# Kernel tuning notes

Measured on AMD Instinct MI355X. Metric: run time of the kernel, lower is better.

Reference implementation:

```python
import jax, jax.numpy as jnp
import numpy as np

B, H, S, D = 2, 16, 2048, 64  # depth = dmodel / num_heads
DMODEL = H * D


def setup_inputs() -> dict:
    key = jax.random.key(0)
    kq, kk, kv, kw = jax.random.split(key, 4)
    Q = jax.random.normal(kq, (B, H, S, D), dtype=jnp.float32)
    K = jax.random.normal(kk, (B, H, S, D), dtype=jnp.float32)
    V = jax.random.normal(kv, (B, H, S, D), dtype=jnp.float32)
    W = jax.random.normal(kw, (DMODEL, DMODEL), dtype=jnp.float32) * (1.0 / np.sqrt(DMODEL))
    b = jnp.zeros((DMODEL,), dtype=jnp.float32)
    return {"Q": Q, "K": K, "V": V, "W": W, "b": b}


def reference(Q, K, V, W, b):
    depth = Q.shape[-1]
    # scores: (B, H, S, S) -- full score matrix, matching the original math
    scores = jnp.einsum('bhqd,bhkd->bhqk', Q, K) / jnp.sqrt(jnp.float32(depth))
    attn = jax.nn.softmax(scores, axis=-1)
    vals = jnp.einsum('bhqk,bhkd->bhqd', attn, V)          # (B, H, S, D)
    vals = jnp.transpose(vals, (0, 2, 1, 3))               # (B, S, H, D)
    concat = vals.reshape(vals.shape[0], vals.shape[1], -1)  # (B, S, dmodel)
    return concat @ W + b
```

## Files before the change

kernel.cpp:

```cpp
#include <hip/hip_runtime.h>
#include <hip/hip_bf16.h>


typedef float  f32x16 __attribute__((ext_vector_type(16)));
typedef float  f32x4v __attribute__((ext_vector_type(4)));
typedef float  f32x2v __attribute__((ext_vector_type(2)));
typedef __bf16 bf16x8 __attribute__((ext_vector_type(8)));
typedef __bf16 bf16x4 __attribute__((ext_vector_type(4)));
typedef __bf16 bf16x2 __attribute__((ext_vector_type(2)));

static constexpr int Bn = 2, Hn = 16, Sn = 2048, Dn = 64, DM = 1024;
static constexpr size_t QKV_ELEMS = (size_t)Bn * Hn * Sn * Dn;

#define QSCALE 0.18033688011112042f

#define LGKM_BARRIER() do {                                  \
    asm volatile("s_waitcnt lgkmcnt(0)" ::: "memory");       \
    __builtin_amdgcn_s_barrier();                            \
  } while (0)

#if __has_builtin(__builtin_amdgcn_cvt_pk_bf16_f32)
static __device__ __forceinline__ unsigned pack2(float a, float b) {
  bf16x2 t = __builtin_amdgcn_cvt_pk_bf16_f32(a, b);
  union { bf16x2 v; unsigned u; } c; c.v = t; return c.u;
}
#else
static __device__ __forceinline__ unsigned pack2(float a, float b) {
  union { __bf16 h; unsigned short s; } ua, ub;
  ua.h = (__bf16)a; ub.h = (__bf16)b;
  return (unsigned)ua.s | ((unsigned)ub.s << 16);
}
#endif

static __device__ __forceinline__ void unzip8(const unsigned* wds, bf16x8* r0, bf16x8* r1) {
  union { unsigned u[4]; bf16x8 v; } a, b;
#pragma unroll
  for (int i = 0; i < 4; ++i) {
    unsigned lo = wds[2 * i], hi = wds[2 * i + 1];
    a.u[i] = (lo & 0xffffu) | (hi << 16);
    b.u[i] = (lo >> 16) | (hi & 0xffff0000u);
  }
  *r0 = a.v; *r1 = b.v;
}

__global__ __launch_bounds__(256) void convert_vw(
    const float* __restrict__ v, const float* __restrict__ w,
    __bf16* __restrict__ vt, __bf16* __restrict__ wt) {
  __shared__ __bf16 T[64][74];
  const int bid = blockIdx.x, t = threadIdx.x;

  const float* s0;
  __bf16* dst0 = nullptr;
  int nt_ = 0, kt_ = 0;
  const bool isW = (bid >= 1024);
  {
    const int r = t >> 2, c0 = (t & 3) * 16;
    if (!isW) {
      const int idx = bid;
      const int kv0 = (idx & 31) * 64, bh = idx >> 5;
      s0 = v + ((size_t)bh * Sn + kv0 + r) * Dn + c0;
      dst0 = vt + (size_t)bh * Dn * Sn + kv0;
    } else {
      const int idx = bid - 1024;
      nt_ = (idx & 15) * 64; kt_ = (idx >> 4) * 64;
      s0 = w + (size_t)(kt_ + r) * DM + nt_ + c0;
    }
    union { bf16x8 v8; unsigned u[4]; } o0, o1;
#pragma unroll
    for (int i = 0; i < 2; ++i) {
      f32x4v f = *(const f32x4v*)(s0 + i * 4);
#pragma unroll
      for (int j = 0; j < 4; ++j) o0.v8[i * 4 + j] = (__bf16)f[j];
    }
#pragma unroll
    for (int i = 0; i < 2; ++i) {
      f32x4v f = *(const f32x4v*)(s0 + 8 + i * 4);
#pragma unroll
      for (int j = 0; j < 4; ++j) o1.v8[i * 4 + j] = (__bf16)f[j];
    }
#pragma unroll
    for (int j = 0; j < 4; ++j) {
      *(unsigned*)&T[r][c0 + 2 * j]     = o0.u[j];
      *(unsigned*)&T[r][c0 + 8 + 2 * j] = o1.u[j];
    }
  }
  __syncthreads();
  const int rp = t >> 3, k0 = (t & 7) * 8;
  unsigned wds[8];
#pragma unroll
  for (int i = 0; i < 8; ++i) wds[i] = *(const unsigned*)&T[k0 + i][2 * rp];
  bf16x8 r0, r1; unzip8(wds, &r0, &r1);
  if (!isW) {
    __bf16* d0 = dst0 + (size_t)(2 * rp) * Sn + k0;
    *(bf16x8*)d0 = r0;
    *(bf16x8*)(d0 + Sn) = r1;
  } else {
    const int n0 = nt_ + 2 * rp;
    __bf16* d0 = wt + ((size_t)(n0 >> 5) * 128 + (kt_ >> 3) + (t & 7)) * 256
                    + (n0 & 31) * 8;
    *(bf16x8*)d0 = r0;
    *(bf16x8*)(d0 + 8) = r1;
  }
}

__global__ __launch_bounds__(512, 4) void attn(
    const float* __restrict__ Qf, const float* __restrict__ Kf,
    const __bf16* __restrict__ Vtg, __bf16* __restrict__ Cc, int bz) {
  const int tid = threadIdx.x;
  const int wave = tid >> 6, lane = tid & 63;
  const int ln = lane & 31, g = lane >> 5;
  const int qg = wave >> 1, kh = wave & 1;
  const int f = blockIdx.x;
  const int swz = (f & 7) * 32 + (f >> 3);
  const int qb = swz & 15, h = swz >> 4;

  __shared__ __bf16 Ks[2][128][72];
  __shared__ __bf16 Vs[2][64][136];

  const size_t hoff = (size_t)(bz * Hn + h) * Sn * Dn;
  const float*  Qp = Qf + hoff + (size_t)(qb * 128 + qg * 32) * Dn;
  const float*  Kp = Kf + hoff;
  const __bf16* Vp = Vtg + hoff;

  bf16x8 qf[4];
#pragma unroll
  for (int ks = 0; ks < 4; ++ks) {
    const float* qp = Qp + (size_t)ln * Dn + ks * 16 + g * 8;
    f32x4v f0 = *(const f32x4v*)qp;
    f32x4v f1 = *(const f32x4v*)(qp + 4);
#pragma unroll
    for (int j = 0; j < 4; ++j) {
      qf[ks][j]     = (__bf16)(f0[j] * QSCALE);
      qf[ks][4 + j] = (__bf16)(f1[j] * QSCALE);
    }
  }

  const int kr = tid >> 2, kc = (tid & 3) * 16;
  const int vr = tid >> 3, vc = (tid & 7) * 16;
  const float*  kbasef = Kp + (size_t)kr * Dn + kc;
  const __bf16* vbase  = Vp + (size_t)vr * Sn + vc;

  f32x4v ka0, ka1, ka2, ka3;
  bf16x8 v0r, v1r;
  {
    ka0 = *(const f32x4v*)(kbasef);
    ka1 = *(const f32x4v*)(kbasef + 4);
    ka2 = *(const f32x4v*)(kbasef + 8);
    ka3 = *(const f32x4v*)(kbasef + 12);
    bf16x8 kx0, kx1;
#pragma unroll
    for (int j = 0; j < 4; ++j) {
      kx0[j] = (__bf16)ka0[j]; kx0[4 + j] = (__bf16)ka1[j];
      kx1[j] = (__bf16)ka2[j]; kx1[4 + j] = (__bf16)ka3[j];
    }
    *(bf16x8*)&Ks[0][kr][kc]     = kx0;
    *(bf16x8*)&Ks[0][kr][kc + 8] = kx1;
    v0r = *(const bf16x8*)vbase; v1r = *(const bf16x8*)(vbase + 8);
    union { bf16x8 v; bf16x4 h[2]; } u0, u1; u0.v = v0r; u1.v = v1r;
    union { bf16x4 h[2]; bf16x8 v; } w0, w1;
    w0.h[0] = u0.h[0]; w0.h[1] = u1.h[0];
    w1.h[0] = u0.h[1]; w1.h[1] = u1.h[1];
    *(bf16x8*)&Vs[0][vr][vc]     = w0.v;
    *(bf16x8*)&Vs[0][vr][vc + 8] = w1.v;
  }
  ka0 = *(const f32x4v*)(kbasef + (size_t)128 * Dn);
  ka1 = *(const f32x4v*)(kbasef + (size_t)128 * Dn + 4);
  ka2 = *(const f32x4v*)(kbasef + (size_t)128 * Dn + 8);
  ka3 = *(const f32x4v*)(kbasef + (size_t)128 * Dn + 12);
  v0r = *(const bf16x8*)(vbase + 128);
  v1r = *(const bf16x8*)(vbase + 128 + 8);
  LGKM_BARRIER();

  f32x16 O0 = {}, O1 = {};
  float Lown = 0.0f;
  constexpr int NT = Sn / 128;

  for (int kt = 0; kt < NT; ++kt) {
    const int buf = kt & 1;

    unsigned w[16];
#pragma unroll
    for (int m = 0; m < 2; ++m) {
      bf16x8 kf[4];
#pragma unroll
      for (int ks = 0; ks < 4; ++ks)
        kf[ks] = *(const bf16x8*)&Ks[buf][kh * 64 + m * 32 + ln][ks * 16 + g * 8];

      f32x16 s = {};
      __builtin_amdgcn_s_setprio(1);
#pragma unroll
      for (int ks = 0; ks < 4; ++ks)
        s = __builtin_amdgcn_mfma_f32_32x32x16_bf16(kf[ks], qf[ks], s, 0, 0, 0);
      __builtin_amdgcn_s_setprio(0);

      float p[16];
#pragma unroll
      for (int r = 0; r < 16; ++r) p[r] = __builtin_amdgcn_exp2f(s[r]);
      f32x2v s2 = {0.0f, 0.0f};
#pragma unroll
      for (int tt = 0; tt < 8; ++tt) { f32x2v t2 = {p[2 * tt], p[2 * tt + 1]}; s2 += t2; }
      Lown += s2[0] + s2[1];
#pragma unroll
      for (int tt = 0; tt < 8; ++tt) w[m * 8 + tt] = pack2(p[2 * tt], p[2 * tt + 1]);
    }

    if (kt + 1 < NT) {
      const int nb = buf ^ 1;
      bf16x8 kx0, kx1;
#pragma unroll
      for (int j = 0; j < 4; ++j) {
        kx0[j] = (__bf16)ka0[j]; kx0[4 + j] = (__bf16)ka1[j];
        kx1[j] = (__bf16)ka2[j]; kx1[4 + j] = (__bf16)ka3[j];
      }
      *(bf16x8*)&Ks[nb][kr][kc]     = kx0;
      *(bf16x8*)&Ks[nb][kr][kc + 8] = kx1;
      union { bf16x8 v; bf16x4 h[2]; } u0, u1; u0.v = v0r; u1.v = v1r;
      union { bf16x4 h[2]; bf16x8 v; } w0, w1;
      w0.h[0] = u0.h[0]; w0.h[1] = u1.h[0];
      w1.h[0] = u0.h[1]; w1.h[1] = u1.h[1];
      *(bf16x8*)&Vs[nb][vr][vc]     = w0.v;
      *(bf16x8*)&Vs[nb][vr][vc + 8] = w1.v;
      if (kt + 2 < NT) {
        const float* kp = kbasef + (size_t)(kt + 2) * 128 * Dn;
        ka0 = *(const f32x4v*)kp;       ka1 = *(const f32x4v*)(kp + 4);
        ka2 = *(const f32x4v*)(kp + 8); ka3 = *(const f32x4v*)(kp + 12);
        const __bf16* vp = vbase + (kt + 2) * 128;
        v0r = *(const bf16x8*)vp; v1r = *(const bf16x8*)(vp + 8);
      }
    }

    __builtin_amdgcn_s_setprio(1);
#pragma unroll
    for (int s4 = 0; s4 < 4; ++s4) {
      const int cb = kh * 64 + s4 * 16 + g * 8;
      bf16x8 vf0 = *(const bf16x8*)&Vs[buf][ln][cb];
      bf16x8 vf1 = *(const bf16x8*)&Vs[buf][32 + ln][cb];
      union { unsigned u[4]; bf16x8 v; } pu;
      pu.u[0] = w[s4 * 4 + 0];
      pu.u[1] = w[s4 * 4 + 1];
      pu.u[2] = w[s4 * 4 + 2];
      pu.u[3] = w[s4 * 4 + 3];
      O0 = __builtin_amdgcn_mfma_f32_32x32x16_bf16(vf0, pu.v, O0, 0, 0, 0);
      O1 = __builtin_amdgcn_mfma_f32_32x32x16_bf16(vf1, pu.v, O1, 0, 0, 0);
    }
    __builtin_amdgcn_s_setprio(0);

    LGKM_BARRIER();
  }

  const float Lred = Lown + __shfl_xor(Lown, 32);
  float* Ex = (float*)Ks;
  const int slot = (qg * 64 + lane) * 36;
  if (kh == 1) {
#pragma unroll
    for (int i = 0; i < 4; ++i) {
      f32x4v t = {O0[4 * i], O0[4 * i + 1], O0[4 * i + 2], O0[4 * i + 3]};
      *(f32x4v*)&Ex[slot + 4 * i] = t;
    }
#pragma unroll
    for (int i = 0; i < 4; ++i) {
      f32x4v t = {O1[4 * i], O1[4 * i + 1], O1[4 * i + 2], O1[4 * i + 3]};
      *(f32x4v*)&Ex[slot + 16 + 4 * i] = t;
    }
    Ex[slot + 32] = Lred;
  }
  __syncthreads();
  __bf16* T = (__bf16*)Vs;
  if (kh == 0) {
    float inv;
#pragma unroll
    for (int i = 0; i < 4; ++i) {
      f32x4v t = *(const f32x4v*)&Ex[slot + 4 * i];
#pragma unroll
      for (int c = 0; c < 4; ++c) O0[4 * i + c] += t[c];
    }
#pragma unroll
    for (int i = 0; i < 4; ++i) {
      f32x4v t = *(const f32x4v*)&Ex[slot + 16 + 4 * i];
#pragma unroll
      for (int c = 0; c < 4; ++c) O1[4 * i + c] += t[c];
    }
    inv = 1.0f / (Lred + Ex[slot + 32]);
#pragma unroll
    for (int dh = 0; dh < 2; ++dh) {
#pragma unroll
      for (int a = 0; a < 4; ++a) {
        const f32x16 O = dh ? O1 : O0;
        bf16x4 t4;
#pragma unroll
        for (int c = 0; c < 4; ++c) t4[c] = (__bf16)(O[4 * a + c] * inv);
        *(bf16x4*)&T[(qg * 32 + ln) * 72 + dh * 32 + 8 * a + 4 * g] = t4;
      }
    }
  }
  __syncthreads();
  const int q0 = qb * 128;
#pragma unroll
  for (int i = 0; i < 2; ++i) {
    const int rq = i * 64 + (tid >> 3);
    const int c8 = (tid & 7) * 8;
    bf16x8 o = *(const bf16x8*)&T[rq * 72 + c8];
    const int m = bz * Sn + q0 + rq;
    const int kg = h * 8 + (tid & 7);
    size_t base = ((size_t)(m >> 5) * 128 + kg) * 256 + (m & 31) * 8;
    *(bf16x8*)&Cc[base] = o;
  }
}

__global__ __launch_bounds__(512, 4) void proj(
    const __bf16* __restrict__ A2, const __bf16* __restrict__ Wt2,
    const float* __restrict__ bias, float* __restrict__ out) {
  const int tid = threadIdx.x, wave = tid >> 6, lane = tid & 63;
  const int ln = lane & 31, g = lane >> 5;
  const int mq = wave >> 1, nh = wave & 1;
  const int f = blockIdx.x;
  const int idx = f >> 3;
  const int bn = idx & 15;
  const int bm = (f & 7) * 4 + (idx >> 4);

  const int mg = bm * 4 + mq;
  const int ng = bn * 2 + nh;
  const __bf16* Ab = A2  + (size_t)mg * 128 * 256 + (size_t)ln * 8;
  const __bf16* Wb = Wt2 + (size_t)ng * 128 * 256 + (size_t)ln * 8;

  f32x16 acc = {};
#pragma unroll 4
  for (int kt = 0; kt < 16; ++kt) {
#pragma unroll
    for (int ks = 0; ks < 4; ++ks) {
      const size_t off = (size_t)(kt * 8 + ks * 2 + g) * 256;
      bf16x8 af = *(const bf16x8*)(Ab + off);
      bf16x8 wf = *(const bf16x8*)(Wb + off);
      acc = __builtin_amdgcn_mfma_f32_32x32x16_bf16(af, wf, acc, 0, 0, 0);
    }
  }
  const float bv = bias[bn * 64 + nh * 32 + ln];
#pragma unroll
  for (int r = 0; r < 16; ++r) {
    int row = bm * 128 + mq * 32 + (r & 3) + 8 * (r >> 2) + 4 * g;
    out[(size_t)row * DM + bn * 64 + nh * 32 + ln] = acc[r] + bv;
  }
}

extern "C" void kernel_launch(void* const* d_in, const int* in_sizes, int n_in,
                              void* d_out, int out_size, void* d_ws, size_t ws_size,
                              hipStream_t stream) {
  const float* Q = (const float*)d_in[0];
  const float* K = (const float*)d_in[1];
  const float* V = (const float*)d_in[2];
  const float* W = (const float*)d_in[3];
  const float* b = (const float*)d_in[4];
  float* out = (float*)d_out;

  __bf16* ws  = (__bf16*)d_ws;
  __bf16* Vtg = ws;
  __bf16* Cc  = Vtg + QKV_ELEMS;
  __bf16* Wt  = Cc + QKV_ELEMS;

  convert_vw<<<dim3(1280, 1, 1), 256, 0, stream>>>(V, W, Vtg, Wt);
  attn<<<dim3(256, 1, 1), 512, 0, stream>>>(Q, K, Vtg, Cc, 0);
  attn<<<dim3(256, 1, 1), 512, 0, stream>>>(Q, K, Vtg, Cc, 1);
  proj<<<dim3(512, 1, 1), 512, 0, stream>>>(Cc, Wt, b, out);
}
```

Measured before the change: 165.1 us.

## Process two query sub-tiles per wave and merge batch launches into one grid

Each wave now computes two 32-row query sub-tiles against the same K/V fragments read from LDS. The block shrinks to 256 threads (4 waves) while still covering 128 queries, so each K and V LDS load is reused across twice as many queries. The two per-batch attention launches become a single 512-block launch with the batch index taken from the block index, removing one launch and its tail. In exchange each wave holds more accumulators and Q fragments, so register pressure rises and occupancy may fall (launch bounds change to 256,2).

```diff
diff --git a/kernel.cpp b/kernel.cpp
--- a/kernel.cpp
+++ b/kernel.cpp
@@ -103,129 +103,156 @@
   }
 }
 
-__global__ __launch_bounds__(512, 4) void attn(
+__global__ __launch_bounds__(256, 2) void attn(
     const float* __restrict__ Qf, const float* __restrict__ Kf,
-    const __bf16* __restrict__ Vtg, __bf16* __restrict__ Cc, int bz) {
+    const __bf16* __restrict__ Vtg, __bf16* __restrict__ Cc) {
   const int tid = threadIdx.x;
   const int wave = tid >> 6, lane = tid & 63;
   const int ln = lane & 31, g = lane >> 5;
   const int qg = wave >> 1, kh = wave & 1;
   const int f = blockIdx.x;
-  const int swz = (f & 7) * 32 + (f >> 3);
-  const int qb = swz & 15, h = swz >> 4;
+  const int swz = (f & 7) * 64 + (f >> 3);
+  const int qb = swz & 15, h = (swz >> 4) & 15, bz = swz >> 8;
 
   __shared__ __bf16 Ks[2][128][72];
   __shared__ __bf16 Vs[2][64][136];
 
   const size_t hoff = (size_t)(bz * Hn + h) * Sn * Dn;
-  const float*  Qp = Qf + hoff + (size_t)(qb * 128 + qg * 32) * Dn;
+  const float*  Qp = Qf + hoff + (size_t)(qb * 128 + qg * 64) * Dn;
   const float*  Kp = Kf + hoff;
   const __bf16* Vp = Vtg + hoff;
 
-  bf16x8 qf[4];
-#pragma unroll
-  for (int ks = 0; ks < 4; ++ks) {
-    const float* qp = Qp + (size_t)ln * Dn + ks * 16 + g * 8;
-    f32x4v f0 = *(const f32x4v*)qp;
-    f32x4v f1 = *(const f32x4v*)(qp + 4);
-#pragma unroll
-    for (int j = 0; j < 4; ++j) {
-      qf[ks][j]     = (__bf16)(f0[j] * QSCALE);
-      qf[ks][4 + j] = (__bf16)(f1[j] * QSCALE);
-    }
-  }
-
-  const int kr = tid >> 2, kc = (tid & 3) * 16;
-  const int vr = tid >> 3, vc = (tid & 7) * 16;
-  const float*  kbasef = Kp + (size_t)kr * Dn + kc;
+  bf16x8 qf[2][4];
+#pragma unroll
+  for (int qs = 0; qs < 2; ++qs) {
+#pragma unroll
+    for (int ks = 0; ks < 4; ++ks) {
+      const float* qp = Qp + (size_t)(qs * 32 + ln) * Dn + ks * 16 + g * 8;
+      f32x4v f0 = *(const f32x4v*)qp;
+      f32x4v f1 = *(const f32x4v*)(qp + 4);
+#pragma unroll
+      for (int j = 0; j < 4; ++j) {
+        qf[qs][ks][j]     = (__bf16)(f0[j] * QSCALE);
+        qf[qs][ks][4 + j] = (__bf16)(f1[j] * QSCALE);
+      }
+    }
+  }
+
+  const int kra = tid >> 2, kc = (tid & 3) * 16;
+  const int vr  = tid >> 2, vc = (tid & 3) * 32;
+  const float*  kbasef = Kp + (size_t)kra * Dn + kc;
   const __bf16* vbase  = Vp + (size_t)vr * Sn + vc;
 
-  f32x4v ka0, ka1, ka2, ka3;
-  bf16x8 v0r, v1r;
+  f32x4v ka[2][4];
+  bf16x8 vld[4];
+#pragma unroll
+  for (int j = 0; j < 4; ++j) {
+    ka[0][j] = *(const f32x4v*)(kbasef + j * 4);
+    ka[1][j] = *(const f32x4v*)(kbasef + (size_t)64 * Dn + j * 4);
+  }
+#pragma unroll
+  for (int i = 0; i < 4; ++i) vld[i] = *(const bf16x8*)(vbase + i * 8);
   {
-    ka0 = *(const f32x4v*)(kbasef);
-    ka1 = *(const f32x4v*)(kbasef + 4);
-    ka2 = *(const f32x4v*)(kbasef + 8);
-    ka3 = *(const f32x4v*)(kbasef + 12);
-    bf16x8 kx0, kx1;
-#pragma unroll
-    for (int j = 0; j < 4; ++j) {
-      kx0[j] = (__bf16)ka0[j]; kx0[4 + j] = (__bf16)ka1[j];
-      kx1[j] = (__bf16)ka2[j]; kx1[4 + j] = (__bf16)ka3[j];
-    }
-    *(bf16x8*)&Ks[0][kr][kc]     = kx0;
-    *(bf16x8*)&Ks[0][kr][kc + 8] = kx1;
-    v0r = *(const bf16x8*)vbase; v1r = *(const bf16x8*)(vbase + 8);
-    union { bf16x8 v; bf16x4 h[2]; } u0, u1; u0.v = v0r; u1.v = v1r;
-    union { bf16x4 h[2]; bf16x8 v; } w0, w1;
+#pragma unroll
+    for (int r = 0; r < 2; ++r) {
+      bf16x8 kx0, kx1;
+#pragma unroll
+      for (int j = 0; j < 4; ++j) {
+        kx0[j] = (__bf16)ka[r][0][j]; kx0[4 + j] = (__bf16)ka[r][1][j];
+        kx1[j] = (__bf16)ka[r][2][j]; kx1[4 + j] = (__bf16)ka[r][3][j];
+      }
+      *(bf16x8*)&Ks[0][kra + r * 64][kc]     = kx0;
+      *(bf16x8*)&Ks[0][kra + r * 64][kc + 8] = kx1;
+    }
+    union { bf16x8 v; bf16x4 h[2]; } u0, u1, u2, u3;
+    u0.v = vld[0]; u1.v = vld[1]; u2.v = vld[2]; u3.v = vld[3];
+    union { bf16x4 h[2]; bf16x8 v; } w0, w1, w2, w3;
     w0.h[0] = u0.h[0]; w0.h[1] = u1.h[0];
     w1.h[0] = u0.h[1]; w1.h[1] = u1.h[1];
-    *(bf16x8*)&Vs[0][vr][vc]     = w0.v;
-    *(bf16x8*)&Vs[0][vr][vc + 8] = w1.v;
-  }
-  ka0 = *(const f32x4v*)(kbasef + (size_t)128 * Dn);
-  ka1 = *(const f32x4v*)(kbasef + (size_t)128 * Dn + 4);
-  ka2 = *(const f32x4v*)(kbasef + (size_t)128 * Dn + 8);
-  ka3 = *(const f32x4v*)(kbasef + (size_t)128 * Dn + 12);
-  v0r = *(const bf16x8*)(vbase + 128);
-  v1r = *(const bf16x8*)(vbase + 128 + 8);
+    w2.h[0] = u2.h[0]; w2.h[1] = u3.h[0];
+    w3.h[0] = u2.h[1]; w3.h[1] = u3.h[1];
+    *(bf16x8*)&Vs[0][vr][vc]      = w0.v;
+    *(bf16x8*)&Vs[0][vr][vc + 8]  = w1.v;
+    *(bf16x8*)&Vs[0][vr][vc + 16] = w2.v;
+    *(bf16x8*)&Vs[0][vr][vc + 24] = w3.v;
+  }
+#pragma unroll
+  for (int j = 0; j < 4; ++j) {
+    ka[0][j] = *(const f32x4v*)(kbasef + (size_t)128 * Dn + j * 4);
+    ka[1][j] = *(const f32x4v*)(kbasef + (size_t)192 * Dn + j * 4);
+  }
+#pragma unroll
+  for (int i = 0; i < 4; ++i) vld[i] = *(const bf16x8*)(vbase + 128 + i * 8);
   LGKM_BARRIER();
 
-  f32x16 O0 = {}, O1 = {};
-  float Lown = 0.0f;
+  f32x16 O[2][2] = {};
+  float Lown[2] = {0.0f, 0.0f};
   constexpr int NT = Sn / 128;
 
   for (int kt = 0; kt < NT; ++kt) {
     const int buf = kt & 1;
 
-    unsigned w[16];
+    unsigned w[2][16];
 #pragma unroll
     for (int m = 0; m < 2; ++m) {
       bf16x8 kf[4];
 #pragma unroll
       for (int ks = 0; ks < 4; ++ks)
         kf[ks] = *(const bf16x8*)&Ks[buf][kh * 64 + m * 32 + ln][ks * 16 + g * 8];
-
-      f32x16 s = {};
-      __builtin_amdgcn_s_setprio(1);
-#pragma unroll
-      for (int ks = 0; ks < 4; ++ks)
-        s = __builtin_amdgcn_mfma_f32_32x32x16_bf16(kf[ks], qf[ks], s, 0, 0, 0);
-      __builtin_amdgcn_s_setprio(0);
-
-      float p[16];
-#pragma unroll
-      for (int r = 0; r < 16; ++r) p[r] = __builtin_amdgcn_exp2f(s[r]);
-      f32x2v s2 = {0.0f, 0.0f};
-#pragma unroll
-      for (int tt = 0; tt < 8; ++tt) { f32x2v t2 = {p[2 * tt], p[2 * tt + 1]}; s2 += t2; }
-      Lown += s2[0] + s2[1];
-#pragma unroll
-      for (int tt = 0; tt < 8; ++tt) w[m * 8 + tt] = pack2(p[2 * tt], p[2 * tt + 1]);
+#pragma unroll
+      for (int qs = 0; qs < 2; ++qs) {
+        f32x16 s = {};
+        __builtin_amdgcn_s_setprio(1);
+#pragma unroll
+        for (int ks = 0; ks < 4; ++ks)
+          s = __builtin_amdgcn_mfma_f32_32x32x16_bf16(kf[ks], qf[qs][ks], s, 0, 0, 0);
+        __builtin_amdgcn_s_setprio(0);
+        float p[16];
+#pragma unroll
+        for (int r = 0; r < 16; ++r) p[r] = __builtin_amdgcn_exp2f(s[r]);
+        f32x2v s2 = {0.0f, 0.0f};
+#pragma unroll
+        for (int tt = 0; tt < 8; ++tt) { f32x2v t2 = {p[2 * tt], p[2 * tt + 1]}; s2 += t2; }
+        Lown[qs] += s2[0] + s2[1];
+#pragma unroll
+        for (int tt = 0; tt < 8; ++tt) w[qs][m * 8 + tt] = pack2(p[2 * tt], p[2 * tt + 1]);
+      }
     }
 
     if (kt + 1 < NT) {
       const int nb = buf ^ 1;
-      bf16x8 kx0, kx1;
-#pragma unroll
-      for (int j = 0; j < 4; ++j) {
-        kx0[j] = (__bf16)ka0[j]; kx0[4 + j] = (__bf16)ka1[j];
-        kx1[j] = (__bf16)ka2[j]; kx1[4 + j] = (__bf16)ka3[j];
-      }
-      *(bf16x8*)&Ks[nb][kr][kc]     = kx0;
-      *(bf16x8*)&Ks[nb][kr][kc + 8] = kx1;
-      union { bf16x8 v; bf16x4 h[2]; } u0, u1; u0.v = v0r; u1.v = v1r;
-      union { bf16x4 h[2]; bf16x8 v; } w0, w1;
+#pragma unroll
+      for (int r = 0; r < 2; ++r) {
+        bf16x8 kx0, kx1;
+#pragma unroll
+        for (int j = 0; j < 4; ++j) {
+          kx0[j] = (__bf16)ka[r][0][j]; kx0[4 + j] = (__bf16)ka[r][1][j];
+          kx1[j] = (__bf16)ka[r][2][j]; kx1[4 + j] = (__bf16)ka[r][3][j];
+        }
+        *(bf16x8*)&Ks[nb][kra + r * 64][kc]     = kx0;
+        *(bf16x8*)&Ks[nb][kra + r * 64][kc + 8] = kx1;
+      }
+      union { bf16x8 v; bf16x4 h[2]; } u0, u1, u2, u3;
+      u0.v = vld[0]; u1.v = vld[1]; u2.v = vld[2]; u3.v = vld[3];
+      union { bf16x4 h[2]; bf16x8 v; } w0, w1, w2, w3;
       w0.h[0] = u0.h[0]; w0.h[1] = u1.h[0];
       w1.h[0] = u0.h[1]; w1.h[1] = u1.h[1];
-      *(bf16x8*)&Vs[nb][vr][vc]     = w0.v;
-      *(bf16x8*)&Vs[nb][vr][vc + 8] = w1.v;
+      w2.h[0] = u2.h[0]; w2.h[1] = u3.h[0];
+      w3.h[0] = u2.h[1]; w3.h[1] = u3.h[1];
+      *(bf16x8*)&Vs[nb][vr][vc]      = w0.v;
+      *(bf16x8*)&Vs[nb][vr][vc + 8]  = w1.v;
+      *(bf16x8*)&Vs[nb][vr][vc + 16] = w2.v;
+      *(bf16x8*)&Vs[nb][vr][vc + 24] = w3.v;
       if (kt + 2 < NT) {
         const float* kp = kbasef + (size_t)(kt + 2) * 128 * Dn;
-        ka0 = *(const f32x4v*)kp;       ka1 = *(const f32x4v*)(kp + 4);
-        ka2 = *(const f32x4v*)(kp + 8); ka3 = *(const f32x4v*)(kp + 12);
+#pragma unroll
+        for (int j = 0; j < 4; ++j) {
+          ka[0][j] = *(const f32x4v*)(kp + j * 4);
+          ka[1][j] = *(const f32x4v*)(kp + (size_t)64 * Dn + j * 4);
+        }
         const __bf16* vp = vbase + (kt + 2) * 128;
-        v0r = *(const bf16x8*)vp; v1r = *(const bf16x8*)(vp + 8);
+#pragma unroll
+        for (int i = 0; i < 4; ++i) vld[i] = *(const bf16x8*)(vp + i * 8);
       }
     }
 
@@ -235,69 +262,79 @@
       const int cb = kh * 64 + s4 * 16 + g * 8;
       bf16x8 vf0 = *(const bf16x8*)&Vs[buf][ln][cb];
       bf16x8 vf1 = *(const bf16x8*)&Vs[buf][32 + ln][cb];
-      union { unsigned u[4]; bf16x8 v; } pu;
-      pu.u[0] = w[s4 * 4 + 0];
-      pu.u[1] = w[s4 * 4 + 1];
-      pu.u[2] = w[s4 * 4 + 2];
-      pu.u[3] = w[s4 * 4 + 3];
-      O0 = __builtin_amdgcn_mfma_f32_32x32x16_bf16(vf0, pu.v, O0, 0, 0, 0);
-      O1 = __builtin_amdgcn_mfma_f32_32x32x16_bf16(vf1, pu.v, O1, 0, 0, 0);
+#pragma unroll
+      for (int qs = 0; qs < 2; ++qs) {
+        union { unsigned u[4]; bf16x8 v; } pu;
+        pu.u[0] = w[qs][s4 * 4 + 0];
+        pu.u[1] = w[qs][s4 * 4 + 1];
+        pu.u[2] = w[qs][s4 * 4 + 2];
+        pu.u[3] = w[qs][s4 * 4 + 3];
+        O[qs][0] = __builtin_amdgcn_mfma_f32_32x32x16_bf16(vf0, pu.v, O[qs][0], 0, 0, 0);
+        O[qs][1] = __builtin_amdgcn_mfma_f32_32x32x16_bf16(vf1, pu.v, O[qs][1], 0, 0, 0);
+      }
     }
     __builtin_amdgcn_s_setprio(0);
 
     LGKM_BARRIER();
   }
 
-  const float Lred = Lown + __shfl_xor(Lown, 32);
+  float Lred[2];
+  Lred[0] = Lown[0] + __shfl_xor(Lown[0], 32);
+  Lred[1] = Lown[1] + __shfl_xor(Lown[1], 32);
   float* Ex = (float*)Ks;
-  const int slot = (qg * 64 + lane) * 36;
   if (kh == 1) {
 #pragma unroll
-    for (int i = 0; i < 4; ++i) {
-      f32x4v t = {O0[4 * i], O0[4 * i + 1], O0[4 * i + 2], O0[4 * i + 3]};
-      *(f32x4v*)&Ex[slot + 4 * i] = t;
-    }
-#pragma unroll
-    for (int i = 0; i < 4; ++i) {
-      f32x4v t = {O1[4 * i], O1[4 * i + 1], O1[4 * i + 2], O1[4 * i + 3]};
-      *(f32x4v*)&Ex[slot + 16 + 4 * i] = t;
-    }
-    Ex[slot + 32] = Lred;
+    for (int qs = 0; qs < 2; ++qs) {
+      const int slot = ((qg * 2 + qs) * 64 + lane) * 36;
+#pragma unroll
+      for (int i = 0; i < 4; ++i) {
+        f32x4v t = {O[qs][0][4 * i], O[qs][0][4 * i + 1], O[qs][0][4 * i + 2], O[qs][0][4 * i + 3]};
+        *(f32x4v*)&Ex[slot + 4 * i] = t;
+      }
+#pragma unroll
+      for (int i = 0; i < 4; ++i) {
+        f32x4v t = {O[qs][1][4 * i], O[qs][1][4 * i + 1], O[qs][1][4 * i + 2], O[qs][1][4 * i + 3]};
+        *(f32x4v*)&Ex[slot + 16 + 4 * i] = t;
+      }
+      Ex[slot + 32] = Lred[qs];
+    }
   }
   __syncthreads();
   __bf16* T = (__bf16*)Vs;
   if (kh == 0) {
-    float inv;
-#pragma unroll
-    for (int i = 0; i < 4; ++i) {
-      f32x4v t = *(const f32x4v*)&Ex[slot + 4 * i];
-#pragma unroll
-      for (int c = 0; c < 4; ++c) O0[4 * i + c] += t[c];
-    }
-#pragma unroll
-    for (int i = 0; i < 4; ++i) {
-      f32x4v t = *(const f32x4v*)&Ex[slot + 16 + 4 * i];
-#pragma unroll
-      for (int c = 0; c < 4; ++c) O1[4 * i + c] += t[c];
-    }
-    inv = 1.0f / (Lred + Ex[slot + 32]);
-#pragma unroll
-    for (int dh = 0; dh < 2; ++dh) {
-#pragma unroll
-      for (int a = 0; a < 4; ++a) {
-        const f32x16 O = dh ? O1 : O0;
-        bf16x4 t4;
-#pragma unroll
-        for (int c = 0; c < 4; ++c) t4[c] = (__bf16)(O[4 * a + c] * inv);
-        *(bf16x4*)&T[(qg * 32 + ln) * 72 + dh * 32 + 8 * a + 4 * g] = t4;
+#pragma unroll
+    for (int qs = 0; qs < 2; ++qs) {
+      const int slot = ((qg * 2 + qs) * 64 + lane) * 36;
+#pragma unroll
+      for (int i = 0; i < 4; ++i) {
+        f32x4v t = *(const f32x4v*)&Ex[slot + 4 * i];
+#pragma unroll
+        for (int c = 0; c < 4; ++c) O[qs][0][4 * i + c] += t[c];
+      }
+#pragma unroll
+      for (int i = 0; i < 4; ++i) {
+        f32x4v t = *(const f32x4v*)&Ex[slot + 16 + 4 * i];
+#pragma unroll
+        for (int c = 0; c < 4; ++c) O[qs][1][4 * i + c] += t[c];
+      }
+      const float inv = 1.0f / (Lred[qs] + Ex[slot + 32]);
+#pragma unroll
+      for (int dh = 0; dh < 2; ++dh) {
+#pragma unroll
+        for (int a = 0; a < 4; ++a) {
+          bf16x4 t4;
+#pragma unroll
+          for (int c = 0; c < 4; ++c) t4[c] = (__bf16)(O[qs][dh][4 * a + c] * inv);
+          *(bf16x4*)&T[((qg * 2 + qs) * 32 + ln) * 72 + dh * 32 + 8 * a + 4 * g] = t4;
+        }
       }
     }
   }
   __syncthreads();
   const int q0 = qb * 128;
 #pragma unroll
-  for (int i = 0; i < 2; ++i) {
-    const int rq = i * 64 + (tid >> 3);
+  for (int i = 0; i < 4; ++i) {
+    const int rq = i * 32 + (tid >> 3);
     const int c8 = (tid & 7) * 8;
     bf16x8 o = *(const bf16x8*)&T[rq * 72 + c8];
     const int m = bz * Sn + q0 + rq;
@@ -358,7 +395,6 @@
   __bf16* Wt  = Cc + QKV_ELEMS;
 
   convert_vw<<<dim3(1280, 1, 1), 256, 0, stream>>>(V, W, Vtg, Wt);
-  attn<<<dim3(256, 1, 1), 512, 0, stream>>>(Q, K, Vtg, Cc, 0);
-  attn<<<dim3(256, 1, 1), 512, 0, stream>>>(Q, K, Vtg, Cc, 1);
+  attn<<<dim3(512, 1, 1), 256, 0, stream>>>(Q, K, Vtg, Cc);
   proj<<<dim3(512, 1, 1), 512, 0, stream>>>(Cc, Wt, b, out);
 }
```

Result: no change. 166.4 us (+0.8%).

## Merge batch launches into one 1024-thread attention kernel with four-way key split

Applied to the files above, without the earlier changes.

The two per-batch attention launches become a single launch of 512 blocks, each with 1024 threads (16 waves). Within a block the key tile is split four ways instead of two, so each wave handles 32 keys per tile. Partial outputs and row sums are combined with a two-step tree reduction through shared memory. Next-tile staging now loads directly after the PV step instead of prefetching two tiles ahead in registers. This aims to cut launch overhead and raise wave-level parallelism, at the cost of more reduction barriers, less latency hiding on global loads and higher shared memory use per block.

```diff
diff --git a/kernel.cpp b/kernel.cpp
--- a/kernel.cpp
+++ b/kernel.cpp
@@ -103,19 +103,20 @@
   }
 }
 
-__global__ __launch_bounds__(512, 4) void attn(
+__global__ __launch_bounds__(1024, 8) void attn(
     const float* __restrict__ Qf, const float* __restrict__ Kf,
-    const __bf16* __restrict__ Vtg, __bf16* __restrict__ Cc, int bz) {
+    const __bf16* __restrict__ Vtg, __bf16* __restrict__ Cc) {
+  __shared__ __align__(16) unsigned char lds[71680];
+  __bf16 (*Ks)[128][72]  = (__bf16 (*)[128][72])lds;
+  __bf16 (*Vs)[64][136]  = (__bf16 (*)[64][136])(lds + 36864);
+
   const int tid = threadIdx.x;
   const int wave = tid >> 6, lane = tid & 63;
   const int ln = lane & 31, g = lane >> 5;
-  const int qg = wave >> 1, kh = wave & 1;
+  const int qg = wave >> 2, kh = wave & 3;
   const int f = blockIdx.x;
-  const int swz = (f & 7) * 32 + (f >> 3);
-  const int qb = swz & 15, h = swz >> 4;
-
-  __shared__ __bf16 Ks[2][128][72];
-  __shared__ __bf16 Vs[2][64][136];
+  const int swz = (f & 7) * 64 + (f >> 3);
+  const int qb = swz & 15, h = (swz >> 4) & 15, bz = swz >> 8;
 
   const size_t hoff = (size_t)(bz * Hn + h) * Sn * Dn;
   const float*  Qp = Qf + hoff + (size_t)(qb * 128 + qg * 32) * Dn;
@@ -135,40 +136,29 @@
     }
   }
 
-  const int kr = tid >> 2, kc = (tid & 3) * 16;
-  const int vr = tid >> 3, vc = (tid & 7) * 16;
-  const float*  kbasef = Kp + (size_t)kr * Dn + kc;
-  const __bf16* vbase  = Vp + (size_t)vr * Sn + vc;
-
-  f32x4v ka0, ka1, ka2, ka3;
-  bf16x8 v0r, v1r;
-  {
-    ka0 = *(const f32x4v*)(kbasef);
-    ka1 = *(const f32x4v*)(kbasef + 4);
-    ka2 = *(const f32x4v*)(kbasef + 8);
-    ka3 = *(const f32x4v*)(kbasef + 12);
-    bf16x8 kx0, kx1;
-#pragma unroll
-    for (int j = 0; j < 4; ++j) {
-      kx0[j] = (__bf16)ka0[j]; kx0[4 + j] = (__bf16)ka1[j];
-      kx1[j] = (__bf16)ka2[j]; kx1[4 + j] = (__bf16)ka3[j];
-    }
-    *(bf16x8*)&Ks[0][kr][kc]     = kx0;
-    *(bf16x8*)&Ks[0][kr][kc + 8] = kx1;
-    v0r = *(const bf16x8*)vbase; v1r = *(const bf16x8*)(vbase + 8);
-    union { bf16x8 v; bf16x4 h[2]; } u0, u1; u0.v = v0r; u1.v = v1r;
-    union { bf16x4 h[2]; bf16x8 v; } w0, w1;
-    w0.h[0] = u0.h[0]; w0.h[1] = u1.h[0];
-    w1.h[0] = u0.h[1]; w1.h[1] = u1.h[1];
-    *(bf16x8*)&Vs[0][vr][vc]     = w0.v;
-    *(bf16x8*)&Vs[0][vr][vc + 8] = w1.v;
-  }
-  ka0 = *(const f32x4v*)(kbasef + (size_t)128 * Dn);
-  ka1 = *(const f32x4v*)(kbasef + (size_t)128 * Dn + 4);
-  ka2 = *(const f32x4v*)(kbasef + (size_t)128 * Dn + 8);
-  ka3 = *(const f32x4v*)(kbasef + (size_t)128 * Dn + 12);
-  v0r = *(const bf16x8*)(vbase + 128);
-  v1r = *(const bf16x8*)(vbase + 128 + 8);
+  const int kr = tid >> 3, kc = (tid & 7) * 8;
+  const int vr = tid >> 4, vc = (tid & 15) * 8;
+  const float*  kbase = Kp + (size_t)kr * Dn + kc;
+  const __bf16* vbase = Vp + (size_t)vr * Sn + vc;
+  const int voff = (vc >> 4) * 16 + ((vc & 8) ? 4 : 0);
+
+#define STAGE(b, t) do {                                          \
+    const float* kp_ = kbase + (size_t)(t) * 128 * Dn;            \
+    f32x4v a0_ = *(const f32x4v*)kp_;                             \
+    f32x4v a1_ = *(const f32x4v*)(kp_ + 4);                       \
+    bf16x8 vl_ = *(const bf16x8*)(vbase + (t) * 128);             \
+    bf16x8 kx_;                                                   \
+    _Pragma("unroll")                                             \
+    for (int j_ = 0; j_ < 4; ++j_) {                              \
+      kx_[j_] = (__bf16)a0_[j_]; kx_[4 + j_] = (__bf16)a1_[j_];   \
+    }                                                             \
+    *(bf16x8*)&Ks[b][kr][kc] = kx_;                               \
+    union { bf16x8 v; bf16x4 h[2]; } uv_; uv_.v = vl_;            \
+    *(bf16x4*)&Vs[b][vr][voff]     = uv_.h[0];                    \
+    *(bf16x4*)&Vs[b][vr][voff + 8] = uv_.h[1];                    \
+  } while (0)
+
+  STAGE(0, 0);
   LGKM_BARRIER();
 
   f32x16 O0 = {}, O1 = {};
@@ -178,61 +168,32 @@
   for (int kt = 0; kt < NT; ++kt) {
     const int buf = kt & 1;
 
-    unsigned w[16];
-#pragma unroll
-    for (int m = 0; m < 2; ++m) {
-      bf16x8 kf[4];
-#pragma unroll
-      for (int ks = 0; ks < 4; ++ks)
-        kf[ks] = *(const bf16x8*)&Ks[buf][kh * 64 + m * 32 + ln][ks * 16 + g * 8];
-
-      f32x16 s = {};
-      __builtin_amdgcn_s_setprio(1);
-#pragma unroll
-      for (int ks = 0; ks < 4; ++ks)
-        s = __builtin_amdgcn_mfma_f32_32x32x16_bf16(kf[ks], qf[ks], s, 0, 0, 0);
-      __builtin_amdgcn_s_setprio(0);
-
-      float p[16];
-#pragma unroll
-      for (int r = 0; r < 16; ++r) p[r] = __builtin_amdgcn_exp2f(s[r]);
-      f32x2v s2 = {0.0f, 0.0f};
-#pragma unroll
-      for (int tt = 0; tt < 8; ++tt) { f32x2v t2 = {p[2 * tt], p[2 * tt + 1]}; s2 += t2; }
-      Lown += s2[0] + s2[1];
-#pragma unroll
-      for (int tt = 0; tt < 8; ++tt) w[m * 8 + tt] = pack2(p[2 * tt], p[2 * tt + 1]);
-    }
-
-    if (kt + 1 < NT) {
-      const int nb = buf ^ 1;
-      bf16x8 kx0, kx1;
-#pragma unroll
-      for (int j = 0; j < 4; ++j) {
-        kx0[j] = (__bf16)ka0[j]; kx0[4 + j] = (__bf16)ka1[j];
-        kx1[j] = (__bf16)ka2[j]; kx1[4 + j] = (__bf16)ka3[j];
-      }
-      *(bf16x8*)&Ks[nb][kr][kc]     = kx0;
-      *(bf16x8*)&Ks[nb][kr][kc + 8] = kx1;
-      union { bf16x8 v; bf16x4 h[2]; } u0, u1; u0.v = v0r; u1.v = v1r;
-      union { bf16x4 h[2]; bf16x8 v; } w0, w1;
-      w0.h[0] = u0.h[0]; w0.h[1] = u1.h[0];
-      w1.h[0] = u0.h[1]; w1.h[1] = u1.h[1];
-      *(bf16x8*)&Vs[nb][vr][vc]     = w0.v;
-      *(bf16x8*)&Vs[nb][vr][vc + 8] = w1.v;
-      if (kt + 2 < NT) {
-        const float* kp = kbasef + (size_t)(kt + 2) * 128 * Dn;
-        ka0 = *(const f32x4v*)kp;       ka1 = *(const f32x4v*)(kp + 4);
-        ka2 = *(const f32x4v*)(kp + 8); ka3 = *(const f32x4v*)(kp + 12);
-        const __bf16* vp = vbase + (kt + 2) * 128;
-        v0r = *(const bf16x8*)vp; v1r = *(const bf16x8*)(vp + 8);
-      }
-    }
-
+    bf16x8 kf[4];
+#pragma unroll
+    for (int ks = 0; ks < 4; ++ks)
+      kf[ks] = *(const bf16x8*)&Ks[buf][kh * 32 + ln][ks * 16 + g * 8];
+    f32x16 s = {};
     __builtin_amdgcn_s_setprio(1);
 #pragma unroll
-    for (int s4 = 0; s4 < 4; ++s4) {
-      const int cb = kh * 64 + s4 * 16 + g * 8;
+    for (int ks = 0; ks < 4; ++ks)
+      s = __builtin_amdgcn_mfma_f32_32x32x16_bf16(kf[ks], qf[ks], s, 0, 0, 0);
+    __builtin_amdgcn_s_setprio(0);
+
+    float p[16];
+#pragma unroll
+    for (int r = 0; r < 16; ++r) p[r] = __builtin_amdgcn_exp2f(s[r]);
+    f32x2v s2 = {0.0f, 0.0f};
+#pragma unroll
+    for (int tt = 0; tt < 8; ++tt) { f32x2v t2 = {p[2 * tt], p[2 * tt + 1]}; s2 += t2; }
+    Lown += s2[0] + s2[1];
+    unsigned w[8];
+#pragma unroll
+    for (int tt = 0; tt < 8; ++tt) w[tt] = pack2(p[2 * tt], p[2 * tt + 1]);
+
+    __builtin_amdgcn_s_setprio(1);
+#pragma unroll
+    for (int s4 = 0; s4 < 2; ++s4) {
+      const int cb = kh * 32 + s4 * 16 + g * 8;
       bf16x8 vf0 = *(const bf16x8*)&Vs[buf][ln][cb];
       bf16x8 vf1 = *(const bf16x8*)&Vs[buf][32 + ln][cb];
       union { unsigned u[4]; bf16x8 v; } pu;
@@ -245,42 +206,85 @@
     }
     __builtin_amdgcn_s_setprio(0);
 
+    if (kt + 1 < NT) STAGE(buf ^ 1, kt + 1);
+
     LGKM_BARRIER();
   }
 
-  const float Lred = Lown + __shfl_xor(Lown, 32);
-  float* Ex = (float*)Ks;
-  const int slot = (qg * 64 + lane) * 36;
-  if (kh == 1) {
-#pragma unroll
-    for (int i = 0; i < 4; ++i) {
-      f32x4v t = {O0[4 * i], O0[4 * i + 1], O0[4 * i + 2], O0[4 * i + 3]};
-      *(f32x4v*)&Ex[slot + 4 * i] = t;
-    }
-#pragma unroll
-    for (int i = 0; i < 4; ++i) {
-      f32x4v t = {O1[4 * i], O1[4 * i + 1], O1[4 * i + 2], O1[4 * i + 3]};
-      *(f32x4v*)&Ex[slot + 16 + 4 * i] = t;
-    }
-    Ex[slot + 32] = Lred;
-  }
-  __syncthreads();
-  __bf16* T = (__bf16*)Vs;
+  float Lred = Lown + __shfl_xor(Lown, 32);
+  float* Ex = (float*)lds;
+  float* Lx = (float*)(lds + 65536);
+  {
+    const int idx = ((qg << 1) | (kh >> 1)) * 64 + lane;
+    const int sl = idx * 32;
+    if (kh & 1) {
+#pragma unroll
+      for (int i = 0; i < 4; ++i) {
+        f32x4v t = {O0[4 * i], O0[4 * i + 1], O0[4 * i + 2], O0[4 * i + 3]};
+        *(f32x4v*)&Ex[sl + 4 * i] = t;
+      }
+#pragma unroll
+      for (int i = 0; i < 4; ++i) {
+        f32x4v t = {O1[4 * i], O1[4 * i + 1], O1[4 * i + 2], O1[4 * i + 3]};
+        *(f32x4v*)&Ex[sl + 16 + 4 * i] = t;
+      }
+      Lx[idx] = Lred;
+    }
+    __syncthreads();
+    if (!(kh & 1)) {
+#pragma unroll
+      for (int i = 0; i < 4; ++i) {
+        f32x4v t = *(const f32x4v*)&Ex[sl + 4 * i];
+#pragma unroll
+        for (int c = 0; c < 4; ++c) O0[4 * i + c] += t[c];
+      }
+#pragma unroll
+      for (int i = 0; i < 4; ++i) {
+        f32x4v t = *(const f32x4v*)&Ex[sl + 16 + 4 * i];
+#pragma unroll
+        for (int c = 0; c < 4; ++c) O1[4 * i + c] += t[c];
+      }
+      Lred += Lx[idx];
+    }
+    __syncthreads();
+  }
+  float inv = 0.0f;
+  {
+    const int idx = qg * 64 + lane;
+    const int sl = idx * 32;
+    if (kh == 2) {
+#pragma unroll
+      for (int i = 0; i < 4; ++i) {
+        f32x4v t = {O0[4 * i], O0[4 * i + 1], O0[4 * i + 2], O0[4 * i + 3]};
+        *(f32x4v*)&Ex[sl + 4 * i] = t;
+      }
+#pragma unroll
+      for (int i = 0; i < 4; ++i) {
+        f32x4v t = {O1[4 * i], O1[4 * i + 1], O1[4 * i + 2], O1[4 * i + 3]};
+        *(f32x4v*)&Ex[sl + 16 + 4 * i] = t;
+      }
+      Lx[idx] = Lred;
+    }
+    __syncthreads();
+    if (kh == 0) {
+#pragma unroll
+      for (int i = 0; i < 4; ++i) {
+        f32x4v t = *(const f32x4v*)&Ex[sl + 4 * i];
+#pragma unroll
+        for (int c = 0; c < 4; ++c) O0[4 * i + c] += t[c];
+      }
+#pragma unroll
+      for (int i = 0; i < 4; ++i) {
+        f32x4v t = *(const f32x4v*)&Ex[sl + 16 + 4 * i];
+#pragma unroll
+        for (int c = 0; c < 4; ++c) O1[4 * i + c] += t[c];
+      }
+      inv = 1.0f / (Lred + Lx[idx]);
+    }
+    __syncthreads();
+  }
+  __bf16* T = (__bf16*)lds;
   if (kh == 0) {
-    float inv;
-#pragma unroll
-    for (int i = 0; i < 4; ++i) {
-      f32x4v t = *(const f32x4v*)&Ex[slot + 4 * i];
-#pragma unroll
-      for (int c = 0; c < 4; ++c) O0[4 * i + c] += t[c];
-    }
-#pragma unroll
-    for (int i = 0; i < 4; ++i) {
-      f32x4v t = *(const f32x4v*)&Ex[slot + 16 + 4 * i];
-#pragma unroll
-      for (int c = 0; c < 4; ++c) O1[4 * i + c] += t[c];
-    }
-    inv = 1.0f / (Lred + Ex[slot + 32]);
 #pragma unroll
     for (int dh = 0; dh < 2; ++dh) {
 #pragma unroll
@@ -289,22 +293,21 @@
         bf16x4 t4;
 #pragma unroll
         for (int c = 0; c < 4; ++c) t4[c] = (__bf16)(O[4 * a + c] * inv);
-        *(bf16x4*)&T[(qg * 32 + ln) * 72 + dh * 32 + 8 * a + 4 * g] = t4;
+        *(bf16x4*)&T[((qg * 32 + ln)) * 72 + dh * 32 + 8 * a + 4 * g] = t4;
       }
     }
   }
   __syncthreads();
-  const int q0 = qb * 128;
-#pragma unroll
-  for (int i = 0; i < 2; ++i) {
-    const int rq = i * 64 + (tid >> 3);
+  {
+    const int rq = tid >> 3;
     const int c8 = (tid & 7) * 8;
     bf16x8 o = *(const bf16x8*)&T[rq * 72 + c8];
-    const int m = bz * Sn + q0 + rq;
+    const int m = bz * Sn + qb * 128 + rq;
     const int kg = h * 8 + (tid & 7);
     size_t base = ((size_t)(m >> 5) * 128 + kg) * 256 + (m & 31) * 8;
     *(bf16x8*)&Cc[base] = o;
   }
+#undef STAGE
 }
 
 __global__ __launch_bounds__(512, 4) void proj(
@@ -358,7 +361,6 @@
   __bf16* Wt  = Cc + QKV_ELEMS;
 
   convert_vw<<<dim3(1280, 1, 1), 256, 0, stream>>>(V, W, Vtg, Wt);
-  attn<<<dim3(256, 1, 1), 512, 0, stream>>>(Q, K, Vtg, Cc, 0);
-  attn<<<dim3(256, 1, 1), 512, 0, stream>>>(Q, K, Vtg, Cc, 1);
+  attn<<<dim3(512, 1, 1), 1024, 0, stream>>>(Q, K, Vtg, Cc);
   proj<<<dim3(512, 1, 1), 512, 0, stream>>>(Cc, Wt, b, out);
 }
```

Result: slower. 420.6 us (+154.8%).
